# Performance work log

Hardware: AMD Instinct MI355X
Metric: run time of the kernel (lower is better)

## Reference

```python
import math
import jax, jax.numpy as jnp
import numpy as np

B, S, D_IN, D_OUT = 8, 4096, 512, 512
CHUNK = 64
MAX_LR = 0.2        # config.max_memory_lr
MIN_DECAY = 0.5     # config.min_memory_decay
MAX_NORM = 30.0     # config.memory_max_norm
NORM_EPS = 1e-5     # config.norm_eps (used in normalize_for_delta)


def setup_inputs() -> dict:
    key = jax.random.key(0)
    ks = jax.random.split(key, 5)
    x = jax.random.normal(ks[0], (B, S, D_IN), dtype=jnp.float32)
    # M_init: xavier_uniform(gain=0.1) ~ small; use small normal
    M_init = jax.random.normal(ks[1], (D_OUT, D_IN), dtype=jnp.float32) * 0.02
    # hyperparam projections (Linear(d_in, 1)); torch init: zero weight, logit bias.
    # Use small random weights so the data-dependent path is exercised.
    eta_w = jax.random.normal(ks[2], (1, D_IN), dtype=jnp.float32) * 0.01
    eta_b = jnp.full((1,), math.log(0.08 / 0.92), dtype=jnp.float32)   # inv_sig(memory_lr_init)
    alpha_w = jax.random.normal(ks[3], (1, D_IN), dtype=jnp.float32) * 0.01
    alpha_b = jnp.full((1,), math.log(0.85 / 0.15), dtype=jnp.float32)  # inv_sig(memory_decay_init)
    gate_w = jax.random.normal(ks[4], (1, D_IN), dtype=jnp.float32) * 0.01
    gate_b = jnp.full((1,), 2.0, dtype=jnp.float32)
    return {"x": x, "M_init": M_init, "eta_w": eta_w, "eta_b": eta_b,
            "alpha_w": alpha_w, "alpha_b": alpha_b, "gate_w": gate_w, "gate_b": gate_b}


def _forward(x, M_init, eta_w, eta_b, alpha_w, alpha_b, gate_w, gate_b):
    n_chunks = S // CHUNK
    # [n_chunks, B, C, d_in] for scan over chunks
    xc = x.reshape(B, n_chunks, CHUNK, D_IN).transpose(1, 0, 2, 3)
    M0 = jnp.broadcast_to(M_init, (B, D_OUT, D_IN))

    def step(M, chunk):  # M: [B, d_out, d_in], chunk: [B, C, d_in]
        # per-chunk hyperparams (training mode: base logits = 0)
        eta_tok = jax.nn.sigmoid(chunk @ eta_w.T + eta_b) * MAX_LR            # [B,C,1]
        alpha_tok = MIN_DECAY + jax.nn.sigmoid(chunk @ alpha_w.T + alpha_b) * (1.0 - MIN_DECAY)
        eta = eta_tok.mean(axis=1, keepdims=True)    # [B,1,1]
        alpha = alpha_tok.mean(axis=1, keepdims=True)
        # retrieval: chunk @ M^T
        outputs = jnp.einsum('bcd,bod->bco', chunk, M)  # [B,C,d_out]
        # normalized keys (F.normalize: x / max(||x||, eps))
        kn = jnp.linalg.norm(chunk, axis=-1, keepdims=True)
        keys = chunk / jnp.maximum(kn, NORM_EPS)
        k_mean = keys.mean(axis=1)        # [B,d_in]
        v_target = outputs.mean(axis=1)   # [B,d_out]
        # delta rule rank-1 update
        Mk = jnp.einsum('bod,bd->bo', M, k_mean)
        error = v_target - Mk
        update = error[:, :, None] * k_mean[:, None, :]  # [B,d_out,d_in]
        # chunk_scale = min(C/chunk_size, 1) = 1 here
        M_new = alpha * M + eta * update
        gate = jax.nn.sigmoid(k_mean @ gate_w.T + gate_b)[:, :, None]  # [B,1,1]
        M_new = gate * M_new + (1.0 - gate) * M
        # frobenius-norm clamp
        M_norm = jnp.sqrt(jnp.sum(M_new * M_new, axis=(-2, -1), keepdims=True))
        scale = jnp.minimum(MAX_NORM / (M_norm + 1e-6), 1.0)
        return M_new * scale, outputs

    M_fin, outs = jax.lax.scan(step, M0, xc)  # outs: [n_chunks,B,C,d_out]
    out = outs.transpose(1, 0, 2, 3).reshape(B, S, D_OUT)
    return out, M_fin


def reference(x, M_init, eta_w, eta_b, alpha_w, alpha_b, gate_w, gate_b):
    return _forward(x, M_init, eta_w, eta_b, alpha_w, alpha_b, gate_w, gate_b)
```

## Files before the change

### kernel.cpp

```cpp
#include <hip/hip_runtime.h>
#include <math.h>

#define DIN  512
#define DOUT 512
#define CHK  64
#define NCH  64
#define NB   8
#define SEQ  4096

typedef short bh8_t __attribute__((ext_vector_type(8)));
typedef float f32x4 __attribute__((ext_vector_type(4)));

__device__ __forceinline__ float sigmoidf_(float z){ return 1.0f/(1.0f+__expf(-z)); }

__device__ __forceinline__ unsigned short f2bf(float f){
  unsigned u = __float_as_uint(f);
  unsigned r = (u + 0x7fffu + ((u>>16)&1u)) >> 16;
  return (unsigned short)r;
}
__device__ __forceinline__ void store_bf4(unsigned short* p, float4 v){
  uint2 u;
  u.x = (unsigned)f2bf(v.x) | ((unsigned)f2bf(v.y)<<16);
  u.y = (unsigned)f2bf(v.z) | ((unsigned)f2bf(v.w)<<16);
  *(uint2*)p = u;
}

__global__ __launch_bounds__(256) void k0_m0h(const float* __restrict__ M0, unsigned short* __restrict__ M0h){
  int idx = (blockIdx.x*256 + threadIdx.x)*4;
  float4 v = *(const float4*)(M0+idx);
  store_bf4(M0h+idx, v);
}

__global__ __launch_bounds__(256) void k1_stats(
    const float* __restrict__ x,
    const float* __restrict__ eta_w, const float* __restrict__ eta_b,
    const float* __restrict__ alpha_w, const float* __restrict__ alpha_b,
    const float* __restrict__ gate_w, const float* __restrict__ gate_b,
    float* __restrict__ KM, float* __restrict__ Dv, unsigned short* __restrict__ KMh,
    float* __restrict__ C1, float* __restrict__ C2, float* __restrict__ KM2, float* __restrict__ Q)
{
  int j = blockIdx.x, b = blockIdx.y;
  const float* xc = x + ((size_t)b*SEQ + (size_t)j*CHK) * DIN;
  int tid = threadIdx.x;
  int wave = tid >> 6, lane = tid & 63;

  float km_acc[8], xb_acc[8];
#pragma unroll
  for (int k=0;k<8;k++){ km_acc[k]=0.f; xb_acc[k]=0.f; }
  float eta_sum = 0.f, alpha_sum = 0.f;
  float ew[8], aw[8];
#pragma unroll
  for (int k=0;k<8;k++){ ew[k]=eta_w[lane*8+k]; aw[k]=alpha_w[lane*8+k]; }

  for (int tt=0; tt<16; tt++){
    int t = wave*16 + tt;
    const float* xr = xc + (size_t)t*DIN + lane*8;
    float v[8];
#pragma unroll
    for (int k=0;k<8;k++) v[k]=xr[k];
    float pe=0.f, pa=0.f, pn=0.f;
#pragma unroll
    for (int k=0;k<8;k++){ pe += v[k]*ew[k]; pa += v[k]*aw[k]; pn += v[k]*v[k]; }
#pragma unroll
    for (int off=32; off; off>>=1){
      pe += __shfl_xor(pe, off);
      pa += __shfl_xor(pa, off);
      pn += __shfl_xor(pn, off);
    }
    float inv = 1.0f / fmaxf(sqrtf(pn), 1e-5f);
    eta_sum   += sigmoidf_(pe + eta_b[0]);
    alpha_sum += sigmoidf_(pa + alpha_b[0]);
#pragma unroll
    for (int k=0;k<8;k++){ km_acc[k] += v[k]*inv; xb_acc[k] += v[k]; }
  }

  __shared__ float sKM[4][DIN];
  __shared__ float sXB[4][DIN];
  __shared__ float sEA[4][2];
  __shared__ float sred[4][2];
#pragma unroll
  for (int k=0;k<8;k++){ sKM[wave][lane*8+k]=km_acc[k]; sXB[wave][lane*8+k]=xb_acc[k]; }
  if (lane==0){ sEA[wave][0]=eta_sum; sEA[wave][1]=alpha_sum; }
  __syncthreads();

  float gpart=0.f, km2part=0.f;
  float kmv[2], dvv[2];
#pragma unroll
  for (int k=0;k<2;k++){
    int d = tid*2+k;
    float km = (sKM[0][d]+sKM[1][d]+sKM[2][d]+sKM[3][d]) * (1.0f/64.0f);
    float xb = (sXB[0][d]+sXB[1][d]+sXB[2][d]+sXB[3][d]) * (1.0f/64.0f);
    kmv[k]=km; dvv[k]=xb-km;
    gpart  += km * gate_w[d];
    km2part+= km * km;
  }
#pragma unroll
  for (int off=32; off; off>>=1){
    gpart   += __shfl_xor(gpart, off);
    km2part += __shfl_xor(km2part, off);
  }
  if (lane==0){ sred[wave][0]=gpart; sred[wave][1]=km2part; }
  __syncthreads();

  size_t base = ((size_t)b*NCH + j)*DIN;
#pragma unroll
  for (int k=0;k<2;k++){
    int d = tid*2+k;
    KM[base+d]=kmv[k];
    Dv[base+d]=dvv[k];
    KMh[base+d]=f2bf(kmv[k]);
  }
  if (tid==0){
    float gdot = sred[0][0]+sred[1][0]+sred[2][0]+sred[3][0];
    float km2  = sred[0][1]+sred[1][1]+sred[2][1]+sred[3][1];
    float etam = (sEA[0][0]+sEA[1][0]+sEA[2][0]+sEA[3][0]) * (1.0f/64.0f);
    float alpm = (sEA[0][1]+sEA[1][1]+sEA[2][1]+sEA[3][1]) * (1.0f/64.0f);
    float eta   = 0.2f * etam;
    float alpha = 0.5f + 0.5f * alpm;
    float gate  = sigmoidf_(gdot + gate_b[0]);
    float c1 = gate*alpha + 1.0f - gate;
    float c2 = gate*eta;
    C1[b*NCH+j]  = c1;
    C2[b*NCH+j]  = c2;
    KM2[b*NCH+j] = km2;
    Q[b*NCH+j]   = c2/c1;
  }
}

__global__ __launch_bounds__(256) void k2_g0h0(
    const float* __restrict__ KM, const float* __restrict__ Dv,
    const float* __restrict__ M0, float* __restrict__ G0, float* __restrict__ H0)
{
  int j = blockIdx.x, b = blockIdx.y;
  __shared__ float sD[DIN], sK[DIN];
  int tid = threadIdx.x;
  size_t base = ((size_t)b*NCH+j)*DIN;
  for (int d=tid; d<DIN; d+=256){ sD[d]=Dv[base+d]; sK[d]=KM[base+d]; }
  __syncthreads();
  for (int o=tid; o<DOUT; o+=256){
    const float* mr = M0 + (size_t)o*DIN;
    float ag=0.f, ah=0.f;
    for (int d=0; d<DIN; d+=4){
      float4 m = *(const float4*)(mr+d);
      ag += m.x*sD[d] + m.y*sD[d+1] + m.z*sD[d+2] + m.w*sD[d+3];
      ah += m.x*sK[d] + m.y*sK[d+1] + m.z*sK[d+2] + m.w*sK[d+3];
    }
    G0[base+o]=ag; H0[base+o]=ah;
  }
}

__global__ __launch_bounds__(256) void k2b_gram(
    const float* __restrict__ KM, const float* __restrict__ Dv,
    float* __restrict__ KMD, float* __restrict__ KMKM)
{
  int i = blockIdx.x, b = blockIdx.y;
  __shared__ float sKi[DIN];
  int tid = threadIdx.x;
  const float* kmi = KM + ((size_t)b*NCH+i)*DIN;
  for (int d=tid; d<DIN; d+=256) sKi[d]=kmi[d];
  __syncthreads();
  int wave = tid>>6, lane = tid&63;
  for (int j=wave; j<NCH; j+=4){
    const float* dj = Dv + ((size_t)b*NCH+j)*DIN;
    const float* kj = KM + ((size_t)b*NCH+j)*DIN;
    float pd=0.f, pk=0.f;
#pragma unroll
    for (int k=0;k<8;k++){
      int d = lane + k*64;
      pd += sKi[d]*dj[d];
      pk += sKi[d]*kj[d];
    }
#pragma unroll
    for (int off=32; off; off>>=1){ pd += __shfl_xor(pd,off); pk += __shfl_xor(pk,off); }
    if (lane==0){
      KMD [((size_t)b*NCH+i)*NCH + j] = pd;
      KMKM[((size_t)b*NCH+i)*NCH + j] = pk;
    }
  }
}

__global__ __launch_bounds__(512) void k3a_au(
    const float* __restrict__ G0, const float* __restrict__ H0,
    const float* __restrict__ KMD, const float* __restrict__ KMKM,
    const float* __restrict__ Q, float* __restrict__ AU, float* __restrict__ AW)
{
  int b = blockIdx.x, tid = threadIdx.x;
  __shared__ float scM[4096], scW[4096];
  for (int idx=tid; idx<4096; idx+=512){
    int i=idx>>6, jj=idx&63;
    float qv = Q[b*NCH+i];
    scM[idx] = qv*KMD [((size_t)b*NCH+i)*NCH+jj];
    scW[idx] = qv*KMKM[((size_t)b*NCH+i)*NCH+jj];
  }
  __syncthreads();
  float au[NCH];
  size_t gb = (size_t)b*NCH*DIN + tid;
#pragma unroll 64
  for (int j=0;j<NCH;j++){
    float a = G0[gb + (size_t)j*DIN];
    float w = H0[gb + (size_t)j*DIN];
#pragma unroll
    for (int i=0;i<j;i++){
      a += scM[i*64+j]*au[i];
      w += scW[i*64+j]*au[i];
    }
    au[j]=a;
    AU[gb + (size_t)j*DIN] = a;
    AW[gb + (size_t)j*DIN] = w;
  }
}

__global__ __launch_bounds__(256) void k3b_dots(
    const float* __restrict__ AU, const float* __restrict__ AW,
    float* __restrict__ DUW, float* __restrict__ DUU)
{
  int j = blockIdx.x, b = blockIdx.y;
  int tid = threadIdx.x, wave = tid>>6, lane = tid&63;
  size_t base = ((size_t)b*NCH + j)*DIN;
  float s1=0.f, s2=0.f;
  for (int o=tid; o<DIN; o+=256){
    float u = AU[base+o], w = AW[base+o];
    s1 += u*w; s2 += u*u;
  }
#pragma unroll
  for (int off=32; off; off>>=1){ s1+=__shfl_xor(s1,off); s2+=__shfl_xor(s2,off); }
  __shared__ float r1[4], r2[4];
  if (lane==0){ r1[wave]=s1; r2[wave]=s2; }
  __syncthreads();
  if (tid==0){
    DUW[b*NCH+j] = r1[0]+r1[1]+r1[2]+r1[3];
    DUU[b*NCH+j] = r2[0]+r2[1]+r2[2]+r2[3];
  }
}

__global__ __launch_bounds__(256) void k3c_chain(
    const float* __restrict__ M0,
    const float* __restrict__ C1, const float* __restrict__ C2, const float* __restrict__ KM2,
    const float* __restrict__ DUW, const float* __restrict__ DUU, float* __restrict__ P)
{
  int b = blockIdx.x, tid = threadIdx.x, wave = tid>>6, lane = tid&63;
  float f=0.f;
  const float4* m4 = (const float4*)M0;
  for (int i=tid; i<(DOUT*DIN)/4; i+=256){
    float4 v=m4[i];
    f += v.x*v.x + v.y*v.y + v.z*v.z + v.w*v.w;
  }
#pragma unroll
  for (int off=32; off; off>>=1) f += __shfl_xor(f,off);
  __shared__ float rf[4];
  if (lane==0) rf[wave]=f;
  __syncthreads();
  if (tid==0){
    float F = rf[0]+rf[1]+rf[2]+rf[3];
    float p = 1.f;
    P[b*65+0] = 1.f;
    for (int j=0;j<NCH;j++){
      float c1 = C1[b*NCH+j], c2 = C2[b*NCH+j], km2 = KM2[b*NCH+j];
      float uw = p*p*DUW[b*NCH+j];
      float uu = p*p*DUU[b*NCH+j];
      float Fnew = c1*c1*F + 2.f*c1*c2*uw + c2*c2*uu*km2;
      float scale = fminf(30.0f/(sqrtf(Fnew)+1e-6f), 1.0f);
      F = scale*scale*Fnew;
      p = scale*c1*p;
      P[b*65+j+1] = p;
    }
  }
}

__global__ __launch_bounds__(256) void k3d_uqt(
    const float* __restrict__ AU, const float* __restrict__ Q, unsigned short* __restrict__ UQTh)
{
  int og = blockIdx.x, b = blockIdx.y;
  int tid = threadIdx.x;
  for (int it=0; it<16; it++){
    int idx = it*256 + tid;
    int o = og*64 + (idx>>6);
    int i = idx & 63;
    float v = Q[b*NCH+i] * AU[((size_t)b*NCH+i)*DIN + o];
    UQTh[((size_t)b*DOUT + o)*NCH + i] = f2bf(v);
  }
}

__global__ __launch_bounds__(256) void k4s_s(
    const float* __restrict__ x, const unsigned short* __restrict__ KMh,
    unsigned short* __restrict__ Sh)
{
  int tt = blockIdx.x, b = blockIdx.y;
  int tid = threadIdx.x;
  int lane = tid&63, w = tid>>6, m = lane&15, q = lane>>4;
  __shared__ unsigned short As[64*72];
  __shared__ unsigned short Bs[64*72];
  f32x4 acc[4];
  f32x4 z = {0.f,0.f,0.f,0.f};
#pragma unroll
  for (int nf=0;nf<4;nf++) acc[nf]=z;

  const float* xc = x + ((size_t)b*SEQ + (size_t)tt*64)*DIN;
  for (int k0=0;k0<DIN;k0+=64){
    float4 xa[4]; uint4 bb[2];
#pragma unroll
    for (int v=0;v<4;v++){
      int idx=v*256+tid; int row=idx>>4, cc=idx&15;
      xa[v] = *(const float4*)(xc + (size_t)row*DIN + k0 + cc*4);
    }
#pragma unroll
    for (int v=0;v<2;v++){
      int idx=v*256+tid; int il=idx>>3, cc=idx&7;
      bb[v] = *(const uint4*)&KMh[((size_t)b*NCH+il)*DIN + k0 + cc*8];
    }
    __syncthreads();
#pragma unroll
    for (int v=0;v<4;v++){
      int idx=v*256+tid; int row=idx>>4, cc=idx&15;
      store_bf4(&As[row*72 + cc*4], xa[v]);
    }
#pragma unroll
    for (int v=0;v<2;v++){
      int idx=v*256+tid; int il=idx>>3, cc=idx&7;
      *(uint4*)&Bs[il*72 + cc*8] = bb[v];
    }
    __syncthreads();
#pragma unroll
    for (int kk=0;kk<2;kk++){
      bh8_t af = *(bh8_t*)&As[(w*16+m)*72 + kk*32 + q*8];
#pragma unroll
      for (int nf=0;nf<4;nf++){
        bh8_t bf_ = *(bh8_t*)&Bs[(nf*16+m)*72 + kk*32 + q*8];
        acc[nf] = __builtin_amdgcn_mfma_f32_16x16x32_bf16(af, bf_, acc[nf], 0,0,0);
      }
    }
  }
#pragma unroll
  for (int nf=0;nf<4;nf++)
#pragma unroll
    for (int r=0;r<4;r++)
      Sh[((size_t)b*SEQ + (size_t)tt*64 + w*16 + q*4 + r)*NCH + nf*16 + m] = f2bf(acc[nf][r]);
}

__global__ __launch_bounds__(256) void k4_out(
    const float* __restrict__ x, const unsigned short* __restrict__ M0h,
    const unsigned short* __restrict__ Sh, const unsigned short* __restrict__ UQTh,
    const float* __restrict__ P, float* __restrict__ out)
{
  int ot = blockIdx.x, j = blockIdx.y, b = blockIdx.z;
  int tid = threadIdx.x;
  int lane = tid&63, w = tid>>6, m = lane&15, q = lane>>4;
  int O0 = ot*128;
  __shared__ unsigned short lds[64*72 + 128*72];
  unsigned short* As = lds;
  unsigned short* Bs = lds + 64*72;
  f32x4 acc[8];
  f32x4 z = {0.f,0.f,0.f,0.f};
#pragma unroll
  for (int nf=0;nf<8;nf++) acc[nf]=z;

  for (int idx=tid; idx<64*64; idx+=256){
    int t = idx>>6, i = idx&63;
    unsigned short v = (i<j) ? Sh[((size_t)b*SEQ + (size_t)j*64 + t)*NCH + i] : (unsigned short)0;
    As[t*72+i] = v;
  }
#pragma unroll
  for (int v=0; v<4; v++){
    int idx = v*256+tid;
    int ol = idx>>3, cc = idx&7;
    *(uint4*)&Bs[ol*72 + cc*8] = *(const uint4*)&UQTh[((size_t)b*DOUT + O0+ol)*NCH + cc*8];
  }
  __syncthreads();
#pragma unroll
  for (int kk=0;kk<2;kk++){
    bh8_t af = *(bh8_t*)&As[(w*16+m)*72 + kk*32 + q*8];
#pragma unroll
    for (int nf=0;nf<8;nf++){
      bh8_t bf_ = *(bh8_t*)&Bs[(nf*16+m)*72 + kk*32 + q*8];
      acc[nf] = __builtin_amdgcn_mfma_f32_16x16x32_bf16(af, bf_, acc[nf], 0,0,0);
    }
  }

  const float* xc = x + ((size_t)b*SEQ + (size_t)j*64)*DIN;
  for (int k0=0;k0<DIN;k0+=64){
    float4 xa[4]; uint4 bb[4];
#pragma unroll
    for (int v=0;v<4;v++){
      int idx=v*256+tid; int row=idx>>4, cc=idx&15;
      xa[v] = *(const float4*)(xc + (size_t)row*DIN + k0 + cc*4);
    }
#pragma unroll
    for (int v=0;v<4;v++){
      int idx=v*256+tid; int ol=idx>>3, cc=idx&7;
      bb[v] = *(const uint4*)&M0h[(size_t)(O0+ol)*DIN + k0 + cc*8];
    }
    __syncthreads();
#pragma unroll
    for (int v=0;v<4;v++){
      int idx=v*256+tid; int row=idx>>4, cc=idx&15;
      store_bf4(&As[row*72 + cc*4], xa[v]);
    }
#pragma unroll
    for (int v=0;v<4;v++){
      int idx=v*256+tid; int ol=idx>>3, cc=idx&7;
      *(uint4*)&Bs[ol*72 + cc*8] = bb[v];
    }
    __syncthreads();
#pragma unroll
    for (int kk=0;kk<2;kk++){
      bh8_t af = *(bh8_t*)&As[(w*16+m)*72 + kk*32 + q*8];
#pragma unroll
      for (int nf=0;nf<8;nf++){
        bh8_t bf_ = *(bh8_t*)&Bs[(nf*16+m)*72 + kk*32 + q*8];
        acc[nf] = __builtin_amdgcn_mfma_f32_16x16x32_bf16(af, bf_, acc[nf], 0,0,0);
      }
    }
  }

  float p = P[b*65 + j];
#pragma unroll
  for (int nf=0;nf<8;nf++)
#pragma unroll
    for (int r=0;r<4;r++)
      out[((size_t)b*SEQ + (size_t)j*64 + w*16 + q*4 + r)*DOUT + O0 + nf*16 + m] = p*acc[nf][r];
}

__global__ __launch_bounds__(256) void k5_mfin(
    const float* __restrict__ M0, const float* __restrict__ KM,
    const float* __restrict__ AU, const float* __restrict__ P, const float* __restrict__ Q,
    float* __restrict__ Mout)
{
  int ob = blockIdx.x, b = blockIdx.y;
  int tid = threadIdx.x;
  __shared__ float uo[64][8];
  for (int idx=tid; idx<512; idx+=256){
    int i = idx>>3, oo = idx&7;
    uo[i][oo] = Q[b*NCH+i] * AU[((size_t)b*NCH+i)*DOUT + ob*8+oo];
  }
  __syncthreads();
  float p64 = P[b*65+NCH];
  float acc[2][8];
#pragma unroll
  for (int h=0;h<2;h++)
#pragma unroll
    for (int oo=0;oo<8;oo++) acc[h][oo]=0.f;
  int d0 = tid, d1 = tid+256;
  for (int i=0;i<64;i++){
    float k0 = KM[((size_t)b*NCH+i)*DIN + d0];
    float k1 = KM[((size_t)b*NCH+i)*DIN + d1];
#pragma unroll
    for (int oo=0;oo<8;oo++){
      float u = uo[i][oo];
      acc[0][oo] += u*k0;
      acc[1][oo] += u*k1;
    }
  }
#pragma unroll
  for (int oo=0;oo<8;oo++){
    int o = ob*8+oo;
    Mout[((size_t)b*DOUT + o)*DIN + d0] = p64*(M0[(size_t)o*DIN+d0] + acc[0][oo]);
    Mout[((size_t)b*DOUT + o)*DIN + d1] = p64*(M0[(size_t)o*DIN+d1] + acc[1][oo]);
  }
}

extern "C" void kernel_launch(void* const* d_in, const int* in_sizes, int n_in,
                              void* d_out, int out_size, void* d_ws, size_t ws_size,
                              hipStream_t stream) {
  const float* x       = (const float*)d_in[0];
  const float* M0      = (const float*)d_in[1];
  const float* eta_w   = (const float*)d_in[2];
  const float* eta_b   = (const float*)d_in[3];
  const float* alpha_w = (const float*)d_in[4];
  const float* alpha_b = (const float*)d_in[5];
  const float* gate_w  = (const float*)d_in[6];
  const float* gate_b  = (const float*)d_in[7];
  float* out = (float*)d_out;

  float* ws = (float*)d_ws;
  float* KM   = ws;
  float* Dv   = KM   + 262144;
  float* G0   = Dv   + 262144;
  float* H0   = G0   + 262144;
  float* AU   = H0   + 262144;
  float* AW   = AU   + 262144;
  float* KMD  = AW   + 262144;
  float* KMKM = KMD  + 32768;
  float* C1   = KMKM + 32768;
  float* C2   = C1   + 512;
  float* KM2  = C2   + 512;
  float* Q    = KM2  + 512;
  float* DUW  = Q    + 512;
  float* DUU  = DUW  + 512;
  float* P    = DUU  + 512;
  unsigned short* M0h  = (unsigned short*)(P + 1024);
  unsigned short* KMh  = M0h  + 262144;
  unsigned short* Sh   = KMh  + 262144;
  unsigned short* UQTh = Sh   + 2097152;

  k0_m0h<<<dim3(256), 256, 0, stream>>>(M0, M0h);
  k1_stats<<<dim3(NCH, NB), 256, 0, stream>>>(x, eta_w, eta_b, alpha_w, alpha_b,
                                              gate_w, gate_b, KM, Dv, KMh, C1, C2, KM2, Q);
  k2_g0h0<<<dim3(NCH, NB), 256, 0, stream>>>(KM, Dv, M0, G0, H0);
  k2b_gram<<<dim3(NCH, NB), 256, 0, stream>>>(KM, Dv, KMD, KMKM);
  k4s_s<<<dim3(SEQ/64, NB), 256, 0, stream>>>(x, KMh, Sh);
  k3a_au<<<dim3(NB), 512, 0, stream>>>(G0, H0, KMD, KMKM, Q, AU, AW);
  k3b_dots<<<dim3(NCH, NB), 256, 0, stream>>>(AU, AW, DUW, DUU);
  k3c_chain<<<dim3(NB), 256, 0, stream>>>(M0, C1, C2, KM2, DUW, DUU, P);
  k3d_uqt<<<dim3(8, NB), 256, 0, stream>>>(AU, Q, UQTh);
  k4_out<<<dim3(4, NCH, NB), 256, 0, stream>>>(x, M0h, Sh, UQTh, P, out);
  k5_mfin<<<dim3(64, NB), 256, 0, stream>>>(M0, KM, AU, P, Q, out + (size_t)NB*SEQ*DOUT);
}
```

Baseline: 527.9 us.

## Cache bf16 x, fuse AU/AW/dots/UQT kernels, widen output tile to 256

k1_stats now also writes a bf16 copy of x when the workspace is large enough, and the two GEMM kernels (k4s_s, k4_out) read that copy instead of reloading and converting fp32 x. The triangular AU solve is split across two blocks per batch and fused with the AW recurrence, the AU·AW/AU·AU dot reductions and the transposed bf16 UQT write, which removes the AW buffer and two launches. k4_out's output tile widens from 128 to 256 columns, so the x tile is reused across more outputs but each thread holds more accumulators. The bf16 x path depends on ws_size being big enough, and the wider tile may lower occupancy.

```diff
diff --git a/kernel.cpp b/kernel.cpp
--- a/kernel.cpp
+++ b/kernel.cpp
@@ -37,7 +37,8 @@
     const float* __restrict__ alpha_w, const float* __restrict__ alpha_b,
     const float* __restrict__ gate_w, const float* __restrict__ gate_b,
     float* __restrict__ KM, float* __restrict__ Dv, unsigned short* __restrict__ KMh,
-    float* __restrict__ C1, float* __restrict__ C2, float* __restrict__ KM2, float* __restrict__ Q)
+    float* __restrict__ C1, float* __restrict__ C2, float* __restrict__ KM2, float* __restrict__ Q,
+    unsigned short* __restrict__ xh)
 {
   int j = blockIdx.x, b = blockIdx.y;
   const float* xc = x + ((size_t)b*SEQ + (size_t)j*CHK) * DIN;
@@ -58,6 +59,14 @@
     float v[8];
 #pragma unroll
     for (int k=0;k<8;k++) v[k]=xr[k];
+    if (xh){
+      uint4 hv;
+      hv.x = (unsigned)f2bf(v[0]) | ((unsigned)f2bf(v[1])<<16);
+      hv.y = (unsigned)f2bf(v[2]) | ((unsigned)f2bf(v[3])<<16);
+      hv.z = (unsigned)f2bf(v[4]) | ((unsigned)f2bf(v[5])<<16);
+      hv.w = (unsigned)f2bf(v[6]) | ((unsigned)f2bf(v[7])<<16);
+      *(uint4*)&xh[((size_t)b*SEQ + (size_t)j*CHK + t)*DIN + lane*8] = hv;
+    }
     float pe=0.f, pa=0.f, pn=0.f;
 #pragma unroll
     for (int k=0;k<8;k++){ pe += v[k]*ew[k]; pa += v[k]*aw[k]; pn += v[k]*v[k]; }
@@ -179,57 +188,71 @@
   }
 }
 
-__global__ __launch_bounds__(512) void k3a_au(
+__global__ __launch_bounds__(256) void k3a_au(
     const float* __restrict__ G0, const float* __restrict__ H0,
     const float* __restrict__ KMD, const float* __restrict__ KMKM,
-    const float* __restrict__ Q, float* __restrict__ AU, float* __restrict__ AW)
-{
-  int b = blockIdx.x, tid = threadIdx.x;
+    const float* __restrict__ Q, float* __restrict__ AU,
+    unsigned short* __restrict__ UQTh,
+    float* __restrict__ DUW, float* __restrict__ DUU)
+{
+  int half = blockIdx.x, b = blockIdx.y;
+  int tid = threadIdx.x, wave = tid>>6, lane = tid&63;
+  int d = half*256 + tid;
   __shared__ float scM[4096], scW[4096];
-  for (int idx=tid; idx<4096; idx+=512){
+  __shared__ float sq[64];
+  __shared__ float sdots[64][4][2];
+
+  for (int idx=tid; idx<4096; idx+=256){
     int i=idx>>6, jj=idx&63;
     float qv = Q[b*NCH+i];
     scM[idx] = qv*KMD [((size_t)b*NCH+i)*NCH+jj];
     scW[idx] = qv*KMKM[((size_t)b*NCH+i)*NCH+jj];
   }
-  __syncthreads();
+  if (tid<64) sq[tid] = Q[b*NCH+tid];
+  __syncthreads();
+
   float au[NCH];
-  size_t gb = (size_t)b*NCH*DIN + tid;
-#pragma unroll 64
+  size_t gb = (size_t)b*NCH*DOUT + d;
+#pragma unroll
+  for (int j=0;j<NCH;j++) au[j] = G0[gb + (size_t)j*DOUT];
+
+#pragma unroll
   for (int j=0;j<NCH;j++){
-    float a = G0[gb + (size_t)j*DIN];
-    float w = H0[gb + (size_t)j*DIN];
-#pragma unroll
-    for (int i=0;i<j;i++){
-      a += scM[i*64+j]*au[i];
-      w += scW[i*64+j]*au[i];
-    }
+    float a = au[j];
+#pragma unroll
+    for (int i=0;i<j;i++) a += scM[i*64+j]*au[i];
     au[j]=a;
-    AU[gb + (size_t)j*DIN] = a;
-    AW[gb + (size_t)j*DIN] = w;
-  }
-}
-
-__global__ __launch_bounds__(256) void k3b_dots(
-    const float* __restrict__ AU, const float* __restrict__ AW,
-    float* __restrict__ DUW, float* __restrict__ DUU)
-{
-  int j = blockIdx.x, b = blockIdx.y;
-  int tid = threadIdx.x, wave = tid>>6, lane = tid&63;
-  size_t base = ((size_t)b*NCH + j)*DIN;
-  float s1=0.f, s2=0.f;
-  for (int o=tid; o<DIN; o+=256){
-    float u = AU[base+o], w = AW[base+o];
-    s1 += u*w; s2 += u*u;
-  }
-#pragma unroll
-  for (int off=32; off; off>>=1){ s1+=__shfl_xor(s1,off); s2+=__shfl_xor(s2,off); }
-  __shared__ float r1[4], r2[4];
-  if (lane==0){ r1[wave]=s1; r2[wave]=s2; }
-  __syncthreads();
-  if (tid==0){
-    DUW[b*NCH+j] = r1[0]+r1[1]+r1[2]+r1[3];
-    DUU[b*NCH+j] = r2[0]+r2[1]+r2[2]+r2[3];
+  }
+#pragma unroll
+  for (int j=0;j<NCH;j++) AU[gb + (size_t)j*DOUT] = au[j];
+
+#pragma unroll
+  for (int g=0; g<8; g++){
+    uint4 hv;
+    hv.x = (unsigned)f2bf(au[g*8+0]*sq[g*8+0]) | ((unsigned)f2bf(au[g*8+1]*sq[g*8+1])<<16);
+    hv.y = (unsigned)f2bf(au[g*8+2]*sq[g*8+2]) | ((unsigned)f2bf(au[g*8+3]*sq[g*8+3])<<16);
+    hv.z = (unsigned)f2bf(au[g*8+4]*sq[g*8+4]) | ((unsigned)f2bf(au[g*8+5]*sq[g*8+5])<<16);
+    hv.w = (unsigned)f2bf(au[g*8+6]*sq[g*8+6]) | ((unsigned)f2bf(au[g*8+7]*sq[g*8+7])<<16);
+    *(uint4*)&UQTh[((size_t)b*DOUT + d)*NCH + g*8] = hv;
+  }
+
+#pragma unroll
+  for (int j=0;j<NCH;j++){
+    float w = H0[gb + (size_t)j*DOUT];
+#pragma unroll
+    for (int i=0;i<j;i++) w += scW[i*64+j]*au[i];
+    float s1 = au[j]*w, s2 = au[j]*au[j];
+#pragma unroll
+    for (int off=32; off; off>>=1){ s1+=__shfl_xor(s1,off); s2+=__shfl_xor(s2,off); }
+    if (lane==0){ sdots[j][wave][0]=s1; sdots[j][wave][1]=s2; }
+  }
+  __syncthreads();
+  if (tid<64){
+    int j = tid;
+    float uw = sdots[j][0][0]+sdots[j][1][0]+sdots[j][2][0]+sdots[j][3][0];
+    float uu = sdots[j][0][1]+sdots[j][1][1]+sdots[j][2][1]+sdots[j][3][1];
+    DUW[(b*NCH+j)*2 + half] = uw;
+    DUU[(b*NCH+j)*2 + half] = uu;
   }
 }
 
@@ -256,8 +279,8 @@
     P[b*65+0] = 1.f;
     for (int j=0;j<NCH;j++){
       float c1 = C1[b*NCH+j], c2 = C2[b*NCH+j], km2 = KM2[b*NCH+j];
-      float uw = p*p*DUW[b*NCH+j];
-      float uu = p*p*DUU[b*NCH+j];
+      float uw = p*p*(DUW[(b*NCH+j)*2]+DUW[(b*NCH+j)*2+1]);
+      float uu = p*p*(DUU[(b*NCH+j)*2]+DUU[(b*NCH+j)*2+1]);
       float Fnew = c1*c1*F + 2.f*c1*c2*uw + c2*c2*uu*km2;
       float scale = fminf(30.0f/(sqrtf(Fnew)+1e-6f), 1.0f);
       F = scale*scale*Fnew;
@@ -267,23 +290,10 @@
   }
 }
 
-__global__ __launch_bounds__(256) void k3d_uqt(
-    const float* __restrict__ AU, const float* __restrict__ Q, unsigned short* __restrict__ UQTh)
-{
-  int og = blockIdx.x, b = blockIdx.y;
-  int tid = threadIdx.x;
-  for (int it=0; it<16; it++){
-    int idx = it*256 + tid;
-    int o = og*64 + (idx>>6);
-    int i = idx & 63;
-    float v = Q[b*NCH+i] * AU[((size_t)b*NCH+i)*DIN + o];
-    UQTh[((size_t)b*DOUT + o)*NCH + i] = f2bf(v);
-  }
-}
-
 __global__ __launch_bounds__(256) void k4s_s(
-    const float* __restrict__ x, const unsigned short* __restrict__ KMh,
-    unsigned short* __restrict__ Sh)
+    const float* __restrict__ x, const unsigned short* __restrict__ xh,
+    const unsigned short* __restrict__ KMh,
+    unsigned short* __restrict__ Sh, int use_xh)
 {
   int tt = blockIdx.x, b = blockIdx.y;
   int tid = threadIdx.x;
@@ -295,24 +305,39 @@
 #pragma unroll
   for (int nf=0;nf<4;nf++) acc[nf]=z;
 
-  const float* xc = x + ((size_t)b*SEQ + (size_t)tt*64)*DIN;
   for (int k0=0;k0<DIN;k0+=64){
-    float4 xa[4]; uint4 bb[2];
-#pragma unroll
-    for (int v=0;v<4;v++){
-      int idx=v*256+tid; int row=idx>>4, cc=idx&15;
-      xa[v] = *(const float4*)(xc + (size_t)row*DIN + k0 + cc*4);
-    }
+    uint4 bb[2];
 #pragma unroll
     for (int v=0;v<2;v++){
       int idx=v*256+tid; int il=idx>>3, cc=idx&7;
       bb[v] = *(const uint4*)&KMh[((size_t)b*NCH+il)*DIN + k0 + cc*8];
     }
-    __syncthreads();
-#pragma unroll
-    for (int v=0;v<4;v++){
-      int idx=v*256+tid; int row=idx>>4, cc=idx&15;
-      store_bf4(&As[row*72 + cc*4], xa[v]);
+    if (use_xh){
+      uint4 av[2];
+#pragma unroll
+      for (int v=0;v<2;v++){
+        int idx=v*256+tid; int row=idx>>3, cc=idx&7;
+        av[v] = *(const uint4*)&xh[((size_t)b*SEQ + (size_t)tt*64 + row)*DIN + k0 + cc*8];
+      }
+      __syncthreads();
+#pragma unroll
+      for (int v=0;v<2;v++){
+        int idx=v*256+tid; int row=idx>>3, cc=idx&7;
+        *(uint4*)&As[row*72 + cc*8] = av[v];
+      }
+    } else {
+      float4 xa[4];
+#pragma unroll
+      for (int v=0;v<4;v++){
+        int idx=v*256+tid; int row=idx>>4, cc=idx&15;
+        xa[v] = *(const float4*)(x + ((size_t)b*SEQ + (size_t)tt*64 + row)*DIN + k0 + cc*4);
+      }
+      __syncthreads();
+#pragma unroll
+      for (int v=0;v<4;v++){
+        int idx=v*256+tid; int row=idx>>4, cc=idx&15;
+        store_bf4(&As[row*72 + cc*4], xa[v]);
+      }
     }
 #pragma unroll
     for (int v=0;v<2;v++){
@@ -338,29 +363,28 @@
 }
 
 __global__ __launch_bounds__(256) void k4_out(
-    const float* __restrict__ x, const unsigned short* __restrict__ M0h,
+    const float* __restrict__ x, const unsigned short* __restrict__ xh,
+    const unsigned short* __restrict__ M0h,
     const unsigned short* __restrict__ Sh, const unsigned short* __restrict__ UQTh,
-    const float* __restrict__ P, float* __restrict__ out)
+    const float* __restrict__ P, float* __restrict__ out, int use_xh)
 {
   int ot = blockIdx.x, j = blockIdx.y, b = blockIdx.z;
   int tid = threadIdx.x;
   int lane = tid&63, w = tid>>6, m = lane&15, q = lane>>4;
-  int O0 = ot*128;
-  __shared__ unsigned short lds[64*72 + 128*72];
-  unsigned short* As = lds;
-  unsigned short* Bs = lds + 64*72;
-  f32x4 acc[8];
+  int O0 = ot*256;
+  __shared__ unsigned short As[64*72];
+  __shared__ unsigned short Bs[256*72];
+  f32x4 acc[16];
   f32x4 z = {0.f,0.f,0.f,0.f};
 #pragma unroll
-  for (int nf=0;nf<8;nf++) acc[nf]=z;
+  for (int nf=0;nf<16;nf++) acc[nf]=z;
 
   for (int idx=tid; idx<64*64; idx+=256){
     int t = idx>>6, i = idx&63;
-    unsigned short v = (i<j) ? Sh[((size_t)b*SEQ + (size_t)j*64 + t)*NCH + i] : (unsigned short)0;
-    As[t*72+i] = v;
-  }
-#pragma unroll
-  for (int v=0; v<4; v++){
+    As[t*72+i] = (i<j) ? Sh[((size_t)b*SEQ + (size_t)j*64 + t)*NCH + i] : (unsigned short)0;
+  }
+#pragma unroll
+  for (int v=0; v<8; v++){
     int idx = v*256+tid;
     int ol = idx>>3, cc = idx&7;
     *(uint4*)&Bs[ol*72 + cc*8] = *(const uint4*)&UQTh[((size_t)b*DOUT + O0+ol)*NCH + cc*8];
@@ -370,33 +394,48 @@
   for (int kk=0;kk<2;kk++){
     bh8_t af = *(bh8_t*)&As[(w*16+m)*72 + kk*32 + q*8];
 #pragma unroll
-    for (int nf=0;nf<8;nf++){
+    for (int nf=0;nf<16;nf++){
       bh8_t bf_ = *(bh8_t*)&Bs[(nf*16+m)*72 + kk*32 + q*8];
       acc[nf] = __builtin_amdgcn_mfma_f32_16x16x32_bf16(af, bf_, acc[nf], 0,0,0);
     }
   }
 
-  const float* xc = x + ((size_t)b*SEQ + (size_t)j*64)*DIN;
   for (int k0=0;k0<DIN;k0+=64){
-    float4 xa[4]; uint4 bb[4];
-#pragma unroll
-    for (int v=0;v<4;v++){
-      int idx=v*256+tid; int row=idx>>4, cc=idx&15;
-      xa[v] = *(const float4*)(xc + (size_t)row*DIN + k0 + cc*4);
-    }
-#pragma unroll
-    for (int v=0;v<4;v++){
+    uint4 bb[8];
+#pragma unroll
+    for (int v=0;v<8;v++){
       int idx=v*256+tid; int ol=idx>>3, cc=idx&7;
       bb[v] = *(const uint4*)&M0h[(size_t)(O0+ol)*DIN + k0 + cc*8];
     }
-    __syncthreads();
-#pragma unroll
-    for (int v=0;v<4;v++){
-      int idx=v*256+tid; int row=idx>>4, cc=idx&15;
-      store_bf4(&As[row*72 + cc*4], xa[v]);
-    }
-#pragma unroll
-    for (int v=0;v<4;v++){
+    if (use_xh){
+      uint4 av[2];
+#pragma unroll
+      for (int v=0;v<2;v++){
+        int idx=v*256+tid; int row=idx>>3, cc=idx&7;
+        av[v] = *(const uint4*)&xh[((size_t)b*SEQ + (size_t)j*64 + row)*DIN + k0 + cc*8];
+      }
+      __syncthreads();
+#pragma unroll
+      for (int v=0;v<2;v++){
+        int idx=v*256+tid; int row=idx>>3, cc=idx&7;
+        *(uint4*)&As[row*72 + cc*8] = av[v];
+      }
+    } else {
+      float4 xa[4];
+#pragma unroll
+      for (int v=0;v<4;v++){
+        int idx=v*256+tid; int row=idx>>4, cc=idx&15;
+        xa[v] = *(const float4*)(x + ((size_t)b*SEQ + (size_t)j*64 + row)*DIN + k0 + cc*4);
+      }
+      __syncthreads();
+#pragma unroll
+      for (int v=0;v<4;v++){
+        int idx=v*256+tid; int row=idx>>4, cc=idx&15;
+        store_bf4(&As[row*72 + cc*4], xa[v]);
+      }
+    }
+#pragma unroll
+    for (int v=0;v<8;v++){
       int idx=v*256+tid; int ol=idx>>3, cc=idx&7;
       *(uint4*)&Bs[ol*72 + cc*8] = bb[v];
     }
@@ -405,7 +444,7 @@
     for (int kk=0;kk<2;kk++){
       bh8_t af = *(bh8_t*)&As[(w*16+m)*72 + kk*32 + q*8];
 #pragma unroll
-      for (int nf=0;nf<8;nf++){
+      for (int nf=0;nf<16;nf++){
         bh8_t bf_ = *(bh8_t*)&Bs[(nf*16+m)*72 + kk*32 + q*8];
         acc[nf] = __builtin_amdgcn_mfma_f32_16x16x32_bf16(af, bf_, acc[nf], 0,0,0);
       }
@@ -414,7 +453,7 @@
 
   float p = P[b*65 + j];
 #pragma unroll
-  for (int nf=0;nf<8;nf++)
+  for (int nf=0;nf<16;nf++)
 #pragma unroll
     for (int r=0;r<4;r++)
       out[((size_t)b*SEQ + (size_t)j*64 + w*16 + q*4 + r)*DOUT + O0 + nf*16 + m] = p*acc[nf][r];
@@ -477,31 +516,34 @@
   float* G0   = Dv   + 262144;
   float* H0   = G0   + 262144;
   float* AU   = H0   + 262144;
-  float* AW   = AU   + 262144;
-  float* KMD  = AW   + 262144;
+  float* KMD  = AU   + 262144;
   float* KMKM = KMD  + 32768;
   float* C1   = KMKM + 32768;
   float* C2   = C1   + 512;
   float* KM2  = C2   + 512;
   float* Q    = KM2  + 512;
   float* DUW  = Q    + 512;
-  float* DUU  = DUW  + 512;
-  float* P    = DUU  + 512;
+  float* DUU  = DUW  + 1024;
+  float* P    = DUU  + 1024;
   unsigned short* M0h  = (unsigned short*)(P + 1024);
   unsigned short* KMh  = M0h  + 262144;
   unsigned short* Sh   = KMh  + 262144;
   unsigned short* UQTh = Sh   + 2097152;
+  unsigned short* xh   = UQTh + 262144;
+
+  size_t base_bytes = (size_t)((char*)xh - (char*)d_ws);
+  size_t need_xh = base_bytes + (size_t)16777216*2;
+  int use_xh = (ws_size >= need_xh) ? 1 : 0;
+  unsigned short* xh_arg = use_xh ? xh : (unsigned short*)0;
 
   k0_m0h<<<dim3(256), 256, 0, stream>>>(M0, M0h);
   k1_stats<<<dim3(NCH, NB), 256, 0, stream>>>(x, eta_w, eta_b, alpha_w, alpha_b,
-                                              gate_w, gate_b, KM, Dv, KMh, C1, C2, KM2, Q);
+                                              gate_w, gate_b, KM, Dv, KMh, C1, C2, KM2, Q, xh_arg);
   k2_g0h0<<<dim3(NCH, NB), 256, 0, stream>>>(KM, Dv, M0, G0, H0);
   k2b_gram<<<dim3(NCH, NB), 256, 0, stream>>>(KM, Dv, KMD, KMKM);
-  k4s_s<<<dim3(SEQ/64, NB), 256, 0, stream>>>(x, KMh, Sh);
-  k3a_au<<<dim3(NB), 512, 0, stream>>>(G0, H0, KMD, KMKM, Q, AU, AW);
-  k3b_dots<<<dim3(NCH, NB), 256, 0, stream>>>(AU, AW, DUW, DUU);
+  k4s_s<<<dim3(SEQ/64, NB), 256, 0, stream>>>(x, xh, KMh, Sh, use_xh);
+  k3a_au<<<dim3(2, NB), 256, 0, stream>>>(G0, H0, KMD, KMKM, Q, AU, UQTh, DUW, DUU);
   k3c_chain<<<dim3(NB), 256, 0, stream>>>(M0, C1, C2, KM2, DUW, DUU, P);
-  k3d_uqt<<<dim3(8, NB), 256, 0, stream>>>(AU, Q, UQTh);
-  k4_out<<<dim3(4, NCH, NB), 256, 0, stream>>>(x, M0h, Sh, UQTh, P, out);
+  k4_out<<<dim3(2, NCH, NB), 256, 0, stream>>>(x, xh, M0h, Sh, UQTh, P, out, use_xh);
   k5_mfin<<<dim3(64, NB), 256, 0, stream>>>(M0, KM, AU, P, Q, out + (size_t)NB*SEQ*DOUT);
 }
```

Measured after the change: 511.4 us. 3.1% less time.
